# Performance work log

Hardware: AMD Instinct MI355X
Metric: run time of the kernel (lower is better)

The kernel has to match this reference:

```python
import jax, jax.numpy as jnp
from jax import lax
import numpy as np

B, H, W = 8, 160, 256
C, K = 700, 250
N_BINS = 750
N_HIST, N_JIT = 30, 60
N_FRAMES = N_HIST + N_JIT
MAGIC = 400.0 / (750.0 - 500.0 + 500.0)


def setup_inputs() -> dict:
    key = jax.random.key(0)
    ks = jax.random.split(key, 10)
    n_pix = H * W
    return {
        "batched_image": jax.random.normal(ks[0], (B, H, W), jnp.float32),
        "batched_spikes": jax.random.uniform(ks[1], (B, C, N_BINS), jnp.float32),
        "eye_movements": jax.random.randint(ks[2], (B, N_JIT, 2), 0, 15),
        "time_mask": jax.random.uniform(ks[3], (B, N_BINS - K), jnp.float32),
        "forward_sel": jax.random.randint(ks[4], (B, N_BINS, 2), 0, N_FRAMES),
        "forward_weights": jax.random.uniform(ks[5], (B, N_BINS, 2), jnp.float32),
        # scale filters so the generator signal stays O(1) under exp() nonlinearity
        "stacked_flat_spat_filters": jax.random.normal(ks[6], (C, n_pix), jnp.float32) / np.sqrt(n_pix).astype(np.float32),
        "stacked_timecourse_filters": jax.random.normal(ks[7], (C, K), jnp.float32) / np.sqrt(K).astype(np.float32),
        "precomputed_feedback_gensig": 0.1 * jax.random.normal(ks[8], (B, C, N_BINS - K + 1), jnp.float32),
        "precomputed_history_frames": jax.random.normal(ks[9], (B, N_HIST, C), jnp.float32),
    }


def _jitter(image, eye_movements):
    # image: (B,H,W); eye_movements: (B,F,2) int shifts. Gather with zero fill.
    dy, dx = eye_movements[..., 0], eye_movements[..., 1]
    rows = jnp.arange(H)[None, None, :] + dy[:, :, None]      # (B,F,H)
    cols = jnp.arange(W)[None, None, :] + dx[:, :, None]      # (B,F,W)
    vr = (rows >= 0) & (rows < H)
    vc = (cols >= 0) & (cols < W)
    rc = jnp.clip(rows, 0, H - 1)
    cc = jnp.clip(cols, 0, W - 1)
    bidx = jnp.arange(image.shape[0])[:, None, None, None]
    jit = image[bidx, rc[:, :, :, None], cc[:, :, None, :]]   # (B,F,H,W)
    mask = (vr[:, :, :, None] & vc[:, :, None, :]).astype(image.dtype)
    return jit * mask


def reference(batched_image, batched_spikes, eye_movements, time_mask,
              forward_sel, forward_weights, stacked_flat_spat_filters,
              stacked_timecourse_filters, precomputed_feedback_gensig,
              precomputed_history_frames):
    b = batched_image.shape[0]
    # eye-movement jitter (gather)
    jit = _jitter(batched_image, eye_movements)                       # (B,Fj,H,W)
    jit_flat = jit.reshape(b, -1, H * W)                              # (B,Fj,P)
    spat_j = jnp.einsum('cp,bfp->bfc', stacked_flat_spat_filters, jit_flat)
    spat = jnp.concatenate([precomputed_history_frames, spat_j], axis=1)  # (B,Ftot,C)
    # interval-overlap time upsample: each bin mixes <=2 frames
    t = forward_sel.shape[1]
    gath = jnp.take_along_axis(spat, forward_sel.reshape(b, t * 2, 1), axis=1)
    gath = gath.reshape(b, t, 2, -1)                                  # (B,T,2,C)
    upsampled = jnp.einsum('btjc,btj->bct', gath, forward_weights)    # (B,C,T)
    # grouped (depthwise) conv1d, valid, no flip (cross-correlation like torch)
    time_filt = lax.conv_general_dilated(
        upsampled, stacked_timecourse_filters[:, None, :],
        window_strides=(1,), padding='VALID',
        dimension_numbers=('NCH', 'OIH', 'NCH'), feature_group_count=C)  # (B,C,T-K+1)
    gen_sig = time_filt + precomputed_feedback_gensig
    g = gen_sig[:, :, :-1]
    s = batched_spikes[:, :, K:]
    loss = jnp.exp(g) - s * g                                          # Poisson NLL (unnormed)
    loss = loss * time_mask[:, None, :] * MAGIC
    return jnp.sum(loss, axis=(1, 2))
```

## Files before the change

### kernel.cpp

```cpp
#include <hip/hip_runtime.h>
#include <hip/hip_bf16.h>
#include <math.h>

#define BB    8
#define HH    160
#define WW    256
#define CC    700
#define KK    250
#define NBINS 750
#define NHIST 30
#define NJIT  60
#define NFRM  90
#define PP    (HH*WW)
#define TOUT  500
#define MAGIC (400.0f/750.0f)

#define MPAD   512
#define NPAD   768
#define KPTOT  640
#define KSPLIT 20
#define KPZ    32
#define NSTEP  32
#define BSCALE     64.0f
#define INV_BSCALE (1.0f/64.0f)
#define PA_BLKS (32*80)
#define PB_BLKS (48*80)

typedef __attribute__((ext_vector_type(8))) short short8;
typedef __attribute__((ext_vector_type(4))) float f32x4;

__device__ __forceinline__ unsigned char f2fp8(float x) {
    x = fminf(fmaxf(x, -440.f), 440.f);
    unsigned u = __builtin_bit_cast(unsigned, x);
    unsigned s = (u >> 24) & 0x80u;
    int e = (u >> 23) & 0xFF;
    if (e < 121) return (unsigned char)s;
    unsigned u2 = u + 0x7FFFFu + ((u >> 20) & 1u);
    int e2 = (u2 >> 23) & 0xFF;
    unsigned m = (u2 >> 20) & 7u;
    if (e2 > 135 || (e2 == 135 && m == 7u)) return (unsigned char)(s | 0x7E);
    return (unsigned char)(s | ((unsigned)(e2 - 120) << 3) | m);
}

__device__ __forceinline__ unsigned pk4_fp8(float a, float b, float c, float d) {
#if __has_builtin(__builtin_amdgcn_cvt_pk_fp8_f32)
    int v = __builtin_amdgcn_cvt_pk_fp8_f32(a, b, 0, false);
    v = __builtin_amdgcn_cvt_pk_fp8_f32(c, d, v, true);
    return (unsigned)v;
#else
    return (unsigned)f2fp8(a) | ((unsigned)f2fp8(b) << 8)
         | ((unsigned)f2fp8(c) << 16) | ((unsigned)f2fp8(d) << 24);
#endif
}

__device__ __forceinline__ void gload16(const void* g, void* l) {
    __builtin_amdgcn_global_load_lds(
        (const __attribute__((address_space(1))) unsigned int*)g,
        (__attribute__((address_space(3))) unsigned int*)l, 16, 0, 0);
}

__device__ __forceinline__ int SWZ(int X) { return X ^ (((X >> 8) & 7) << 4); }

__device__ __forceinline__ int FRX(int r, int pl) {
    return ((pl >> 6) << 10) | ((((pl >> 3) & 3) * 16 + r) << 4)
         | (((pl >> 5) & 1) << 3) | (pl & 7);
}

__global__ __launch_bounds__(256) void pack_ab(
    const float* __restrict__ img, const int* __restrict__ eye,
    const float* __restrict__ filt,
    unsigned char* __restrict__ Ap, unsigned char* __restrict__ Bp)
{
    __shared__ unsigned char lds[8192];
    const int t = threadIdx.x, w = t >> 6, l = t & 63;
    const int bid = blockIdx.x;

    if (bid < PA_BLKS) {
        const int mt = bid / 80, ch = bid % 80;
        const int kbase = ch * 512;
        #pragma unroll
        for (int sub = 0; sub < 4; ++sub) {
            int r = sub*4 + w, m = mt*16 + r;
            bool mok = (m < 480);
            int b = 0, dy = 0, dx = 0;
            if (mok) {
                b = m / 60; int f = m % 60;
                dy = eye[(b*NJIT + f)*2 + 0];
                dx = eye[(b*NJIT + f)*2 + 1];
            }
            const float* imgb = img + (size_t)b*PP;
            #pragma unroll
            for (int h = 0; h < 2; ++h) {
                int ir = (kbase >> 8) + h + dy;
                bool ok = mok && (ir < HH);
                const float* rowp = imgb + ir*WW + dx;
                int c0 = 4*l;
                float f0 = (ok && c0+0+dx < WW) ? rowp[c0+0] : 0.f;
                float f1 = (ok && c0+1+dx < WW) ? rowp[c0+1] : 0.f;
                float f2 = (ok && c0+2+dx < WW) ? rowp[c0+2] : 0.f;
                float f3 = (ok && c0+3+dx < WW) ? rowp[c0+3] : 0.f;
                unsigned d = pk4_fp8(f0, f1, f2, f3);
                int X = FRX(r, h*256 + c0);
                *(unsigned*)(lds + SWZ(X)) = d;
            }
        }
        __syncthreads();
        unsigned char* outp = Ap + ((size_t)mt*KPTOT + ch*8)*1024;
        #pragma unroll
        for (int i = 0; i < 2; ++i) {
            int X = i*4096 + t*16;
            short8 v = *(const short8*)(lds + SWZ(X));
            *(short8*)(outp + X) = v;
        }
    } else {
        const int bb = bid - PA_BLKS;
        const int nt = bb / 80, ch = bb % 80;
        const int kbase = ch * 512;
        #pragma unroll
        for (int sub = 0; sub < 4; ++sub) {
            int r = sub*4 + w, n = nt*16 + r;
            float4 va = make_float4(0.f,0.f,0.f,0.f), vb = va;
            if (n < CC) {
                const float* rowp = filt + (size_t)n*PP + kbase;
                va = *(const float4*)(rowp + l*4);
                vb = *(const float4*)(rowp + l*4 + 256);
            }
            unsigned da = pk4_fp8(va.x*BSCALE, va.y*BSCALE, va.z*BSCALE, va.w*BSCALE);
            unsigned db = pk4_fp8(vb.x*BSCALE, vb.y*BSCALE, vb.z*BSCALE, vb.w*BSCALE);
            int Xa = FRX(r, 4*l);
            *(unsigned*)(lds + SWZ(Xa)) = da;
            *(unsigned*)(lds + SWZ(Xa + (4 << 10))) = db;
        }
        __syncthreads();
        unsigned char* outp = Bp + ((size_t)nt*KPTOT + ch*8)*1024;
        #pragma unroll
        for (int i = 0; i < 2; ++i) {
            int X = i*4096 + t*16;
            short8 v = *(const short8*)(lds + SWZ(X));
            *(short8*)(outp + X) = v;
        }
    }
}

__global__ __launch_bounds__(256) void gemm_f8(
    const unsigned char* __restrict__ Ap, const unsigned char* __restrict__ Bp,
    __hip_bfloat16* __restrict__ part)
{
    __shared__ unsigned char As[8192];
    __shared__ unsigned char Bs[8192];

    const int t = threadIdx.x, l = t & 63, w = t >> 6;
    const int mtile = blockIdx.x, ntile = blockIdx.y, z = blockIdx.z;
    const int wr = w >> 1, wc = w & 1;

    f32x4 acc[4][4] = {};

    for (int step = 0; step < NSTEP; ++step) {
        const size_t kp = (size_t)z*KPZ + step;
        const int tb0 = w*2, tb1 = w*2 + 1;
        gload16(Ap + ((size_t)(mtile*8 + tb0)*KPTOT + kp)*1024 + l*16, As + tb0*1024);
        gload16(Ap + ((size_t)(mtile*8 + tb1)*KPTOT + kp)*1024 + l*16, As + tb1*1024);
        gload16(Bp + ((size_t)(ntile*8 + tb0)*KPTOT + kp)*1024 + l*16, Bs + tb0*1024);
        gload16(Bp + ((size_t)(ntile*8 + tb1)*KPTOT + kp)*1024 + l*16, Bs + tb1*1024);
        __syncthreads();

        ulonglong2 a[4], b[4];
        #pragma unroll
        for (int i = 0; i < 4; ++i)
            a[i] = *(const ulonglong2*)(As + (wr*4 + i)*1024 + l*16);
        #pragma unroll
        for (int j = 0; j < 4; ++j)
            b[j] = *(const ulonglong2*)(Bs + (wc*4 + j)*1024 + l*16);
        #pragma unroll
        for (int i = 0; i < 4; ++i)
            #pragma unroll
            for (int j = 0; j < 4; ++j) {
                acc[i][j] = __builtin_amdgcn_mfma_f32_16x16x32_fp8_fp8(
                    (long long)a[i].x, (long long)b[j].x, acc[i][j], 0, 0, 0);
                acc[i][j] = __builtin_amdgcn_mfma_f32_16x16x32_fp8_fp8(
                    (long long)a[i].y, (long long)b[j].y, acc[i][j], 0, 0, 0);
            }
        __syncthreads();
    }

    const int rbase = (l >> 4)*4, cl = l & 15;
    #pragma unroll
    for (int i = 0; i < 4; ++i)
        #pragma unroll
        for (int j = 0; j < 4; ++j) {
            int m = mtile*128 + wr*64 + i*16 + rbase;
            int n = ntile*128 + wc*64 + j*16 + cl;
            __hip_bfloat16* p = part + ((size_t)z*MPAD + m)*NPAD + n;
            #pragma unroll
            for (int r = 0; r < 4; ++r)
                p[(size_t)r*NPAD] = __float2bfloat16(acc[i][j][r]);
        }
}

__global__ __launch_bounds__(256) void build_spat(
    const float* __restrict__ hist, const __hip_bfloat16* __restrict__ part,
    float* __restrict__ spat)
{
    int idx = blockIdx.x*256 + threadIdx.x;
    if (idx >= BB*NFRM*CC) return;
    int c   = idx % CC;
    int rem = idx / CC;
    int fr  = rem % NFRM;
    int b   = rem / NFRM;
    float v;
    if (fr < NHIST) {
        v = hist[(b*NHIST + fr)*CC + c];
    } else {
        int m = b*NJIT + (fr - NHIST);
        v = 0.f;
        #pragma unroll
        for (int kp = 0; kp < KSPLIT; ++kp)
            v += __bfloat162float(part[((size_t)kp*MPAD + m)*NPAD + c]);
        v *= INV_BSCALE;
    }
    spat[idx] = v;
}

__global__ __launch_bounds__(64) void conv_loss(
    const float* __restrict__ spat, const int* __restrict__ sel,
    const float* __restrict__ wts,  const float* __restrict__ tc,
    const float* __restrict__ fb,   const float* __restrict__ spk,
    const float* __restrict__ tmask, float* __restrict__ lpart)
{
    __shared__ float tcs[256];
    __shared__ float ups[864];

    const int lane = threadIdx.x;
    const int c = blockIdx.x;
    const int b = blockIdx.y;

    for (int k = lane; k < 256; k += 64)
        tcs[k] = (k < KK) ? tc[c*KK + k] : 0.f;

    const float* spb = spat + (size_t)b*NFRM*CC + c;
    for (int tt = lane; tt < 768; tt += 64) {
        float v = 0.f;
        if (tt < NBINS) {
            int base = (b*NBINS + tt)*2;
            int s0 = sel[base], s1 = sel[base+1];
            float w0 = wts[base], w1 = wts[base+1];
            v = w0 * spb[s0*CC] + w1 * spb[s1*CC];
        }
        ups[tt + (tt >> 3)] = v;
    }
    __syncthreads();

    const int t0 = lane * 8;
    float u[16];
    #pragma unroll
    for (int j = 0; j < 16; ++j) { int q = t0 + j; u[j] = ups[q + (q >> 3)]; }

    float acc[8] = {};
    #pragma unroll 4
    for (int kc = 0; kc < 248; kc += 8) {
        #pragma unroll
        for (int kk = 0; kk < 8; ++kk) {
            float w2 = tcs[kc + kk];
            #pragma unroll
            for (int j = 0; j < 8; ++j) acc[j] += w2 * u[kk + j];
        }
        #pragma unroll
        for (int j = 0; j < 8; ++j) u[j] = u[j + 8];
        #pragma unroll
        for (int j = 0; j < 8; ++j) {
            int q = t0 + kc + 16 + j;
            u[j + 8] = ups[q + (q >> 3)];
        }
    }
    #pragma unroll
    for (int kk = 0; kk < 8; ++kk) {
        float w2 = tcs[248 + kk];
        #pragma unroll
        for (int j = 0; j < 8; ++j) acc[j] += w2 * u[kk + j];
    }

    const size_t bc = (size_t)b*CC + c;
    const float* fbp = fb  + bc*(TOUT+1);
    const float* sp  = spk + bc*NBINS + KK;
    const float* tm  = tmask + (size_t)b*TOUT;
    float lsum = 0.f;
    #pragma unroll
    for (int j = 0; j < 8; ++j) {
        int tt = t0 + j;
        if (tt < TOUT) {
            float g  = acc[j] + fbp[tt];
            float sv = sp[tt];
            lsum += (__expf(g) - sv*g) * tm[tt];
        }
    }
    #pragma unroll
    for (int off = 32; off > 0; off >>= 1)
        lsum += __shfl_down(lsum, off);
    if (lane == 0) lpart[bc] = lsum * MAGIC;
}

__global__ __launch_bounds__(256) void reduce_out(
    const float* __restrict__ lpart, float* __restrict__ out)
{
    __shared__ float red[256];
    int b = blockIdx.x, t = threadIdx.x;
    float s = 0.f;
    for (int i = t; i < CC; i += 256) s += lpart[(size_t)b*CC + i];
    red[t] = s; __syncthreads();
    for (int o = 128; o > 0; o >>= 1) {
        if (t < o) red[t] += red[t+o];
        __syncthreads();
    }
    if (t == 0) out[b] = red[0];
}

extern "C" void kernel_launch(void* const* d_in, const int* in_sizes, int n_in,
                              void* d_out, int out_size, void* d_ws, size_t ws_size,
                              hipStream_t stream) {
    const float* image = (const float*)d_in[0];
    const float* spk   = (const float*)d_in[1];
    const int*   eye   = (const int*)d_in[2];
    const float* tmask = (const float*)d_in[3];
    const int*   sel   = (const int*)d_in[4];
    const float* wts   = (const float*)d_in[5];
    const float* filt  = (const float*)d_in[6];
    const float* tc    = (const float*)d_in[7];
    const float* fb    = (const float*)d_in[8];
    const float* hist  = (const float*)d_in[9];
    float* out = (float*)d_out;

    unsigned char* Ap = (unsigned char*)d_ws;
    unsigned char* Bp = Ap + (size_t)32*KPTOT*1024;
    __hip_bfloat16* part = (__hip_bfloat16*)(Bp + (size_t)48*KPTOT*1024);
    float* spat  = (float*)(part + (size_t)KSPLIT*MPAD*NPAD);
    float* lpart = spat + (size_t)BB*NFRM*CC;

    pack_ab  <<<dim3(PA_BLKS + PB_BLKS), 256, 0, stream>>>(image, eye, filt, Ap, Bp);
    gemm_f8  <<<dim3(4, 6, KSPLIT), 256, 0, stream>>>(Ap, Bp, part);
    build_spat<<<dim3((BB*NFRM*CC + 255)/256), 256, 0, stream>>>(hist, part, spat);
    conv_loss<<<dim3(CC, BB), 64, 0, stream>>>(spat, sel, wts, tc, fb, spk, tmask, lpart);
    reduce_out<<<dim3(BB), 256, 0, stream>>>(lpart, out);
}
```

Measured before the change: 126.9 us.

## Raise GEMM split-K to 32, remap block order, and coarsen pack blocks

The fp8 GEMM now splits K into 32 slices of 20 steps each instead of 20 slices of 32, launched as a flat 1-D grid with a remapped block-to-(tile, z) order. Each pack block now handles four K chunks in a loop, hoisting the eye-movement lookups and cutting the block count by four. The aim is to fill the GPU more evenly and improve L2 locality, while reducing pack launch overhead. In exchange, the split-K partial buffer grows and the reduction in build_spat has more partials to sum.

```diff
diff --git a/kernel.cpp b/kernel.cpp
--- a/kernel.cpp
+++ b/kernel.cpp
@@ -18,13 +18,12 @@
 #define MPAD   512
 #define NPAD   768
 #define KPTOT  640
-#define KSPLIT 20
-#define KPZ    32
-#define NSTEP  32
+#define KSPLIT 32
+#define KPZ    20
 #define BSCALE     64.0f
 #define INV_BSCALE (1.0f/64.0f)
-#define PA_BLKS (32*80)
-#define PB_BLKS (48*80)
+#define PA_BLKS (32*20)
+#define PB_BLKS (48*20)
 
 typedef __attribute__((ext_vector_type(8))) short short8;
 typedef __attribute__((ext_vector_type(4))) float f32x4;
@@ -76,68 +75,83 @@
     const int bid = blockIdx.x;
 
     if (bid < PA_BLKS) {
-        const int mt = bid / 80, ch = bid % 80;
-        const int kbase = ch * 512;
+        const int mt = bid / 20, ch4 = bid % 20;
+        int rbv[4], rdy[4], rdx[4]; bool rok[4];
         #pragma unroll
         for (int sub = 0; sub < 4; ++sub) {
             int r = sub*4 + w, m = mt*16 + r;
-            bool mok = (m < 480);
+            rok[sub] = (m < 480);
             int b = 0, dy = 0, dx = 0;
-            if (mok) {
+            if (rok[sub]) {
                 b = m / 60; int f = m % 60;
                 dy = eye[(b*NJIT + f)*2 + 0];
                 dx = eye[(b*NJIT + f)*2 + 1];
             }
-            const float* imgb = img + (size_t)b*PP;
-            #pragma unroll
-            for (int h = 0; h < 2; ++h) {
-                int ir = (kbase >> 8) + h + dy;
-                bool ok = mok && (ir < HH);
-                const float* rowp = imgb + ir*WW + dx;
-                int c0 = 4*l;
-                float f0 = (ok && c0+0+dx < WW) ? rowp[c0+0] : 0.f;
-                float f1 = (ok && c0+1+dx < WW) ? rowp[c0+1] : 0.f;
-                float f2 = (ok && c0+2+dx < WW) ? rowp[c0+2] : 0.f;
-                float f3 = (ok && c0+3+dx < WW) ? rowp[c0+3] : 0.f;
-                unsigned d = pk4_fp8(f0, f1, f2, f3);
-                int X = FRX(r, h*256 + c0);
-                *(unsigned*)(lds + SWZ(X)) = d;
-            }
-        }
-        __syncthreads();
-        unsigned char* outp = Ap + ((size_t)mt*KPTOT + ch*8)*1024;
-        #pragma unroll
-        for (int i = 0; i < 2; ++i) {
-            int X = i*4096 + t*16;
-            short8 v = *(const short8*)(lds + SWZ(X));
-            *(short8*)(outp + X) = v;
+            rbv[sub] = b; rdy[sub] = dy; rdx[sub] = dx;
+        }
+        for (int q = 0; q < 4; ++q) {
+            const int ch = ch4*4 + q;
+            const int kbase = ch * 512;
+            #pragma unroll
+            for (int sub = 0; sub < 4; ++sub) {
+                int r = sub*4 + w;
+                const float* imgb = img + (size_t)rbv[sub]*PP;
+                int dx = rdx[sub];
+                #pragma unroll
+                for (int h = 0; h < 2; ++h) {
+                    int ir = (kbase >> 8) + h + rdy[sub];
+                    bool ok = rok[sub] && (ir < HH);
+                    const float* rowp = imgb + ir*WW + dx;
+                    int c0 = 4*l;
+                    float f0 = (ok && c0+0+dx < WW) ? rowp[c0+0] : 0.f;
+                    float f1 = (ok && c0+1+dx < WW) ? rowp[c0+1] : 0.f;
+                    float f2 = (ok && c0+2+dx < WW) ? rowp[c0+2] : 0.f;
+                    float f3 = (ok && c0+3+dx < WW) ? rowp[c0+3] : 0.f;
+                    unsigned d = pk4_fp8(f0, f1, f2, f3);
+                    int X = FRX(r, h*256 + c0);
+                    *(unsigned*)(lds + SWZ(X)) = d;
+                }
+            }
+            __syncthreads();
+            unsigned char* outp = Ap + ((size_t)mt*KPTOT + ch*8)*1024;
+            #pragma unroll
+            for (int i = 0; i < 2; ++i) {
+                int X = i*4096 + t*16;
+                short8 v = *(const short8*)(lds + SWZ(X));
+                *(short8*)(outp + X) = v;
+            }
+            __syncthreads();
         }
     } else {
         const int bb = bid - PA_BLKS;
-        const int nt = bb / 80, ch = bb % 80;
-        const int kbase = ch * 512;
-        #pragma unroll
-        for (int sub = 0; sub < 4; ++sub) {
-            int r = sub*4 + w, n = nt*16 + r;
-            float4 va = make_float4(0.f,0.f,0.f,0.f), vb = va;
-            if (n < CC) {
-                const float* rowp = filt + (size_t)n*PP + kbase;
-                va = *(const float4*)(rowp + l*4);
-                vb = *(const float4*)(rowp + l*4 + 256);
-            }
-            unsigned da = pk4_fp8(va.x*BSCALE, va.y*BSCALE, va.z*BSCALE, va.w*BSCALE);
-            unsigned db = pk4_fp8(vb.x*BSCALE, vb.y*BSCALE, vb.z*BSCALE, vb.w*BSCALE);
-            int Xa = FRX(r, 4*l);
-            *(unsigned*)(lds + SWZ(Xa)) = da;
-            *(unsigned*)(lds + SWZ(Xa + (4 << 10))) = db;
-        }
-        __syncthreads();
-        unsigned char* outp = Bp + ((size_t)nt*KPTOT + ch*8)*1024;
-        #pragma unroll
-        for (int i = 0; i < 2; ++i) {
-            int X = i*4096 + t*16;
-            short8 v = *(const short8*)(lds + SWZ(X));
-            *(short8*)(outp + X) = v;
+        const int nt = bb / 20, ch4 = bb % 20;
+        for (int q = 0; q < 4; ++q) {
+            const int ch = ch4*4 + q;
+            const int kbase = ch * 512;
+            #pragma unroll
+            for (int sub = 0; sub < 4; ++sub) {
+                int r = sub*4 + w, n = nt*16 + r;
+                float4 va = make_float4(0.f,0.f,0.f,0.f), vb = va;
+                if (n < CC) {
+                    const float* rowp = filt + (size_t)n*PP + kbase;
+                    va = *(const float4*)(rowp + l*4);
+                    vb = *(const float4*)(rowp + l*4 + 256);
+                }
+                unsigned da = pk4_fp8(va.x*BSCALE, va.y*BSCALE, va.z*BSCALE, va.w*BSCALE);
+                unsigned db = pk4_fp8(vb.x*BSCALE, vb.y*BSCALE, vb.z*BSCALE, vb.w*BSCALE);
+                int Xa = FRX(r, 4*l);
+                *(unsigned*)(lds + SWZ(Xa)) = da;
+                *(unsigned*)(lds + SWZ(Xa + (4 << 10))) = db;
+            }
+            __syncthreads();
+            unsigned char* outp = Bp + ((size_t)nt*KPTOT + ch*8)*1024;
+            #pragma unroll
+            for (int i = 0; i < 2; ++i) {
+                int X = i*4096 + t*16;
+                short8 v = *(const short8*)(lds + SWZ(X));
+                *(short8*)(outp + X) = v;
+            }
+            __syncthreads();
         }
     }
 }
@@ -150,12 +164,16 @@
     __shared__ unsigned char Bs[8192];
 
     const int t = threadIdx.x, l = t & 63, w = t >> 6;
-    const int mtile = blockIdx.x, ntile = blockIdx.y, z = blockIdx.z;
+    const int bid = blockIdx.x;
+    const int g   = bid >> 3;
+    const int z   = (bid & 7) + 8*(g / 24);
+    const int tt  = g % 24;
+    const int mtile = tt / 6, ntile = tt % 6;
     const int wr = w >> 1, wc = w & 1;
 
     f32x4 acc[4][4] = {};
 
-    for (int step = 0; step < NSTEP; ++step) {
+    for (int step = 0; step < KPZ; ++step) {
         const size_t kp = (size_t)z*KPZ + step;
         const int tb0 = w*2, tb1 = w*2 + 1;
         gload16(Ap + ((size_t)(mtile*8 + tb0)*KPTOT + kp)*1024 + l*16, As + tb0*1024);
@@ -336,7 +354,7 @@
     float* lpart = spat + (size_t)BB*NFRM*CC;
 
     pack_ab  <<<dim3(PA_BLKS + PB_BLKS), 256, 0, stream>>>(image, eye, filt, Ap, Bp);
-    gemm_f8  <<<dim3(4, 6, KSPLIT), 256, 0, stream>>>(Ap, Bp, part);
+    gemm_f8  <<<dim3(8*96), 256, 0, stream>>>(Ap, Bp, part);
     build_spat<<<dim3((BB*NFRM*CC + 255)/256), 256, 0, stream>>>(hist, part, spat);
     conv_loss<<<dim3(CC, BB), 64, 0, stream>>>(spat, sel, wts, tc, fb, spk, tmask, lpart);
     reduce_out<<<dim3(BB), 256, 0, stream>>>(lpart, out);
```

After: 121.0 us. 1.05x faster.
